# Kernel tuning notes

Hardware: AMD Instinct MI355X
Metric: run time of the kernel (lower is better)

The kernel has to match this reference:

```python
import jax, jax.numpy as jnp
import numpy as np

LAMDA = 0.05
TAU = 0.44
MARGIN = 0.05
PD_EPS = 1e-6   # torch F.pairwise_distance default eps
NORM_EPS = 1e-12  # torch F.normalize default eps

B, C = 131072, 256


def setup_inputs() -> dict:
    key = jax.random.key(0)
    k1, k2 = jax.random.split(key)
    inputs = jax.random.normal(k1, (B, C), dtype=jnp.float32)
    labels = jax.random.randint(k2, (B,), 0, C, dtype=jnp.int64)
    return {"inputs": inputs, "labels": labels}


def _hinge_loss(inputs, labels):
    # F.normalize along dim=1: x / max(||x||_2, eps)
    nrm = jnp.sqrt(jnp.sum(inputs * inputs, axis=1, keepdims=True))
    x = inputs / jnp.maximum(nrm, NORM_EPS)
    a, b = x[0::2], x[1::2]            # [B/2, C] each pair (idx, idx+1)
    # F.pairwise_distance(x,y)^2 = sum((x - y + eps)^2)
    d2 = jnp.sum((a - b + PD_EPS) ** 2, axis=1)  # [B/2]
    eq = labels[0::2] == labels[1::2]
    # Faithful to original: l starts at -1 and is STICKY once set to +1
    # (original code never resets l after a matching pair).
    l = jnp.where(jnp.cumsum(eq.astype(jnp.int32)) > 0, 1.0, -1.0)
    loss_hinge = jnp.sum(jax.nn.relu(MARGIN - l * (TAU - d2)))
    return loss_hinge  # scalar (mean of 0-d tensor == itself)


def reference(inputs, labels):
    # cross entropy with mean reduction
    logp = jax.nn.log_softmax(inputs, axis=-1)
    ce = -jnp.mean(jnp.take_along_axis(logp, labels[:, None], axis=1))
    return ce + LAMDA * _hinge_loss(inputs, labels) / 2.0
```

## Files before the change

kernel.cpp:

```cpp
#include <hip/hip_runtime.h>
#include <cstddef>

#define NROWS 131072
#define NCOLS 256
#define NPAIRS 65536
#define PBLK 512
#define PWAVES (PBLK / 64)
#define PAIRS_PER_WAVE 4
#define NBLK (NPAIRS / (PWAVES * PAIRS_PER_WAVE))
#define P0BLK 64



__device__ __forceinline__ float dpp_sum(float x) {
    x += __int_as_float(__builtin_amdgcn_update_dpp(0, __float_as_int(x), 0x121, 0xF, 0xF, false));
    x += __int_as_float(__builtin_amdgcn_update_dpp(0, __float_as_int(x), 0x122, 0xF, 0xF, false));
    x += __int_as_float(__builtin_amdgcn_update_dpp(0, __float_as_int(x), 0x124, 0xF, 0xF, false));
    x += __int_as_float(__builtin_amdgcn_update_dpp(0, __float_as_int(x), 0x128, 0xF, 0xF, false));
    x += __int_as_float(__builtin_amdgcn_update_dpp(0, __float_as_int(x), 0x142, 0xA, 0xF, false));
    x += __int_as_float(__builtin_amdgcn_update_dpp(0, __float_as_int(x), 0x143, 0xC, 0xF, false));
    return x;
}

__device__ __forceinline__ float bcast63(float x) {
    return __int_as_float(__builtin_amdgcn_readlane(__float_as_int(x), 63));
}

__device__ __forceinline__ unsigned dpp_umin(unsigned x) {
    unsigned y;
    y = (unsigned)__builtin_amdgcn_update_dpp((int)x, (int)x, 0x121, 0xF, 0xF, false); x = x < y ? x : y;
    y = (unsigned)__builtin_amdgcn_update_dpp((int)x, (int)x, 0x122, 0xF, 0xF, false); x = x < y ? x : y;
    y = (unsigned)__builtin_amdgcn_update_dpp((int)x, (int)x, 0x124, 0xF, 0xF, false); x = x < y ? x : y;
    y = (unsigned)__builtin_amdgcn_update_dpp((int)x, (int)x, 0x128, 0xF, 0xF, false); x = x < y ? x : y;
    y = (unsigned)__builtin_amdgcn_update_dpp((int)x, (int)x, 0x142, 0xA, 0xF, false); x = x < y ? x : y;
    y = (unsigned)__builtin_amdgcn_update_dpp((int)x, (int)x, 0x143, 0xC, 0xF, false); x = x < y ? x : y;
    return x;
}

__global__ __launch_bounds__(256) void dcnn_p0(const int* __restrict__ labels,
                                               unsigned* __restrict__ minslot) {
    const int t = blockIdx.x * 256 + threadIdx.x;
    const int4* L = reinterpret_cast<const int4*>(labels);
    int4 q0 = L[2 * t];
    int4 q1 = L[2 * t + 1];
    unsigned base = (unsigned)(4 * t);
    unsigned m = 0xFFFFFFFFu;
    if (q0.x == q0.y) m = base;
    if (q0.z == q0.w) { unsigned c = base + 1; m = m < c ? m : c; }
    if (q1.x == q1.y) { unsigned c = base + 2; m = m < c ? m : c; }
    if (q1.z == q1.w) { unsigned c = base + 3; m = m < c ? m : c; }
    m = dpp_umin(m);
    __shared__ unsigned wmin[4];
    if ((threadIdx.x & 63) == 63) wmin[threadIdx.x >> 6] = m;
    __syncthreads();
    if (threadIdx.x == 0) {
        unsigned a = wmin[0] < wmin[1] ? wmin[0] : wmin[1];
        unsigned b = wmin[2] < wmin[3] ? wmin[2] : wmin[3];
        minslot[blockIdx.x] = a < b ? a : b;
    }
}

__global__ __launch_bounds__(PBLK) void dcnn_pair(
    const float* __restrict__ in, const int* __restrict__ labels,
    const unsigned* __restrict__ minslot,
    float* __restrict__ ce_blk, float* __restrict__ h_blk)
{
    const int wave = threadIdx.x >> 6;
    const int lane = threadIdx.x & 63;

    unsigned p0 = dpp_umin(minslot[lane]);
    p0 = (unsigned)__builtin_amdgcn_readlane((int)p0, 63);

    const int wid = blockIdx.x * PWAVES + wave;
    float ce_acc = 0.0f, h_acc = 0.0f;

    #pragma unroll
    for (int i = 0; i < PAIRS_PER_WAVE; ++i) {
        const int p = wid * PAIRS_PER_WAVE + i;
        const float4* rowA = reinterpret_cast<const float4*>(in + (size_t)(2 * p) * NCOLS);
        const float4* rowB = reinterpret_cast<const float4*>(in + (size_t)(2 * p + 1) * NCOLS);
        float4 fa = rowA[lane];
        float4 fb = rowB[lane];
        int2 lab = reinterpret_cast<const int2*>(labels)[p];

        float sep_a = __expf(fa.x) + __expf(fa.y) + __expf(fa.z) + __expf(fa.w);
        float sep_b = __expf(fb.x) + __expf(fb.y) + __expf(fb.z) + __expf(fb.w);
        float ssp_a = fa.x * fa.x + fa.y * fa.y + fa.z * fa.z + fa.w * fa.w;
        float ssp_b = fb.x * fb.x + fb.y * fb.y + fb.z * fb.z + fb.w * fb.w;

        float sea = bcast63(dpp_sum(sep_a));
        float seb = bcast63(dpp_sum(sep_b));
        float ssa = bcast63(dpp_sum(ssp_a));
        float ssb = bcast63(dpp_sum(ssp_b));

        float inva = rsqrtf(ssa);
        float invb = rsqrtf(ssb);

        float dx = fmaf(fa.x, inva, 1e-6f - fb.x * invb);
        float dy = fmaf(fa.y, inva, 1e-6f - fb.y * invb);
        float dz = fmaf(fa.z, inva, 1e-6f - fb.z * invb);
        float dw = fmaf(fa.w, inva, 1e-6f - fb.w * invb);
        float d2p = fmaf(dx, dx, fmaf(dy, dy, fmaf(dz, dz, dw * dw)));
        float d2 = bcast63(dpp_sum(d2p));

        int sla = __builtin_amdgcn_readfirstlane(lab.x);
        int slb = __builtin_amdgcn_readfirstlane(lab.y);
        int ca = sla & 3, cb = slb & 3;
        float va_l = ca == 0 ? fa.x : ca == 1 ? fa.y : ca == 2 ? fa.z : fa.w;
        float vb_l = cb == 0 ? fb.x : cb == 1 ? fb.y : cb == 2 ? fb.z : fb.w;
        float va = __int_as_float(__builtin_amdgcn_readlane(__float_as_int(va_l), sla >> 2));
        float vb = __int_as_float(__builtin_amdgcn_readlane(__float_as_int(vb_l), slb >> 2));

        ce_acc += (__logf(sea) - va) + (__logf(seb) - vb);

        float l = ((unsigned)p >= p0) ? 1.0f : -1.0f;
        h_acc += fmaxf(0.05f - l * (0.44f - d2), 0.0f);
    }

    __shared__ float cep[PWAVES], hp[PWAVES];
    if (lane == 0) { cep[wave] = ce_acc; hp[wave] = h_acc; }
    __syncthreads();
    if (threadIdx.x == 0) {
        float c = 0.0f, h = 0.0f;
        #pragma unroll
        for (int w = 0; w < PWAVES; ++w) { c += cep[w]; h += hp[w]; }
        ce_blk[blockIdx.x] = c;
        h_blk[blockIdx.x] = h;
    }
}

__global__ __launch_bounds__(1024) void dcnn_final(const float* __restrict__ ce_blk,
                                                   const float* __restrict__ h_blk,
                                                   float* __restrict__ out) {
    const int t = threadIdx.x;
    float c = ce_blk[t] + ce_blk[t + 1024];
    float h = h_blk[t] + h_blk[t + 1024];
    c = dpp_sum(c);
    h = dpp_sum(h);
    __shared__ float cs[16], hs[16];
    if ((t & 63) == 63) { cs[t >> 6] = c; hs[t >> 6] = h; }
    __syncthreads();
    if (t == 0) {
        float C = 0.0f, H = 0.0f;
        #pragma unroll
        for (int i = 0; i < 16; ++i) { C += cs[i]; H += hs[i]; }
        out[0] = C * (1.0f / (float)NROWS) + 0.025f * H;
    }
}

extern "C" void kernel_launch(void* const* d_in, const int* in_sizes, int n_in,
                              void* d_out, int out_size, void* d_ws, size_t ws_size,
                              hipStream_t stream) {
    const float* in = (const float*)d_in[0];
    const int* labels = (const int*)d_in[1];
    float* wsf = (float*)d_ws;
    unsigned* minslot = (unsigned*)d_ws;
    float* ce_blk = wsf + 64;
    float* h_blk = wsf + 64 + NBLK;
    float* out = (float*)d_out;

    dcnn_p0<<<P0BLK, 256, 0, stream>>>(labels, minslot);
    dcnn_pair<<<NBLK, PBLK, 0, stream>>>(in, labels, minslot, ce_blk, h_blk);
    dcnn_final<<<1, 1024, 0, stream>>>(ce_blk, h_blk, out);
}
```

Baseline: 195.9 us.

## Split label gather into prelude kernel and use 16-lane groups per pair

Moves the label-logit gather into the first kernel, which now also finds the first matching pair. The main kernel then processes one pair per 16-lane group, cutting each cross-lane reduction from a full-wave DPP plus readlane to a 16-lane DPP reduction. The distance is rewritten via the dot product (2 - 2·cos plus an eps term), so the normalized difference vector is never formed. The price is an extra scattered global read per row, slightly different rounding in d2, and idle lanes in the per-pair scalar tail.

New measurement: 195.7 us. No clear change (-0.1%).

```diff
diff --git a/kernel.cpp b/kernel.cpp
--- a/kernel.cpp
+++ b/kernel.cpp
@@ -4,26 +4,27 @@
 #define NROWS 131072
 #define NCOLS 256
 #define NPAIRS 65536
-#define PBLK 512
-#define PWAVES (PBLK / 64)
-#define PAIRS_PER_WAVE 4
+#define PBLK 256
+#define PWAVES 4
+#define PITER 2
+#define PAIRS_PER_WAVE (4 * PITER)
 #define NBLK (NPAIRS / (PWAVES * PAIRS_PER_WAVE))
-#define P0BLK 64
+#define GBLK 256
 
 
-
-__device__ __forceinline__ float dpp_sum(float x) {
+__device__ __forceinline__ float rsum16(float x) {
     x += __int_as_float(__builtin_amdgcn_update_dpp(0, __float_as_int(x), 0x121, 0xF, 0xF, false));
     x += __int_as_float(__builtin_amdgcn_update_dpp(0, __float_as_int(x), 0x122, 0xF, 0xF, false));
     x += __int_as_float(__builtin_amdgcn_update_dpp(0, __float_as_int(x), 0x124, 0xF, 0xF, false));
     x += __int_as_float(__builtin_amdgcn_update_dpp(0, __float_as_int(x), 0x128, 0xF, 0xF, false));
+    return x;
+}
+
+__device__ __forceinline__ float dpp_sum(float x) {
+    x = rsum16(x);
     x += __int_as_float(__builtin_amdgcn_update_dpp(0, __float_as_int(x), 0x142, 0xA, 0xF, false));
     x += __int_as_float(__builtin_amdgcn_update_dpp(0, __float_as_int(x), 0x143, 0xC, 0xF, false));
     return x;
-}
-
-__device__ __forceinline__ float bcast63(float x) {
-    return __int_as_float(__builtin_amdgcn_readlane(__float_as_int(x), 63));
 }
 
 __device__ __forceinline__ unsigned dpp_umin(unsigned x) {
@@ -37,114 +38,139 @@
     return x;
 }
 
-__global__ __launch_bounds__(256) void dcnn_p0(const int* __restrict__ labels,
-                                               unsigned* __restrict__ minslot) {
-    const int t = blockIdx.x * 256 + threadIdx.x;
-    const int4* L = reinterpret_cast<const int4*>(labels);
-    int4 q0 = L[2 * t];
-    int4 q1 = L[2 * t + 1];
-    unsigned base = (unsigned)(4 * t);
-    unsigned m = 0xFFFFFFFFu;
-    if (q0.x == q0.y) m = base;
-    if (q0.z == q0.w) { unsigned c = base + 1; m = m < c ? m : c; }
-    if (q1.x == q1.y) { unsigned c = base + 2; m = m < c ? m : c; }
-    if (q1.z == q1.w) { unsigned c = base + 3; m = m < c ? m : c; }
+__global__ __launch_bounds__(256) void dcnn_gp0(
+    const float* __restrict__ in, const int* __restrict__ labels,
+    unsigned* __restrict__ minslot, float* __restrict__ ceg)
+{
+    const int p = blockIdx.x * 256 + threadIdx.x;
+    int2 L = reinterpret_cast<const int2*>(labels)[p];
+    float va = in[(size_t)(2 * p) * NCOLS + L.x];
+    float vb = in[(size_t)(2 * p + 1) * NCOLS + L.y];
+    float g = va + vb;
+    unsigned m = (L.x == L.y) ? (unsigned)p : 0xFFFFFFFFu;
+    g = dpp_sum(g);
     m = dpp_umin(m);
-    __shared__ unsigned wmin[4];
-    if ((threadIdx.x & 63) == 63) wmin[threadIdx.x >> 6] = m;
+    __shared__ float gs[4];
+    __shared__ unsigned ms[4];
+    const int lane = threadIdx.x & 63, w = threadIdx.x >> 6;
+    if (lane == 63) { gs[w] = g; ms[w] = m; }
     __syncthreads();
     if (threadIdx.x == 0) {
-        unsigned a = wmin[0] < wmin[1] ? wmin[0] : wmin[1];
-        unsigned b = wmin[2] < wmin[3] ? wmin[2] : wmin[3];
+        ceg[blockIdx.x] = (gs[0] + gs[1]) + (gs[2] + gs[3]);
+        unsigned a = ms[0] < ms[1] ? ms[0] : ms[1];
+        unsigned b = ms[2] < ms[3] ? ms[2] : ms[3];
         minslot[blockIdx.x] = a < b ? a : b;
     }
 }
 
 __global__ __launch_bounds__(PBLK) void dcnn_pair(
-    const float* __restrict__ in, const int* __restrict__ labels,
+    const float* __restrict__ in,
     const unsigned* __restrict__ minslot,
-    float* __restrict__ ce_blk, float* __restrict__ h_blk)
+    float* __restrict__ lse_blk, float* __restrict__ h_blk)
 {
     const int wave = threadIdx.x >> 6;
     const int lane = threadIdx.x & 63;
+    const int g = lane >> 4;
+    const int s = lane & 15;
 
-    unsigned p0 = dpp_umin(minslot[lane]);
-    p0 = (unsigned)__builtin_amdgcn_readlane((int)p0, 63);
+    unsigned m0 = minslot[lane], m1 = minslot[lane + 64];
+    unsigned m2 = minslot[lane + 128], m3 = minslot[lane + 192];
+    unsigned mm = m0 < m1 ? m0 : m1;
+    unsigned mn = m2 < m3 ? m2 : m3;
+    mm = mm < mn ? mm : mn;
+    unsigned p0 = (unsigned)__builtin_amdgcn_readlane((int)dpp_umin(mm), 63);
 
-    const int wid = blockIdx.x * PWAVES + wave;
-    float ce_acc = 0.0f, h_acc = 0.0f;
+    const int wbase = (blockIdx.x * PWAVES + wave) * PAIRS_PER_WAVE;
+    float lse_acc = 0.0f, h_acc = 0.0f;
 
     #pragma unroll
-    for (int i = 0; i < PAIRS_PER_WAVE; ++i) {
-        const int p = wid * PAIRS_PER_WAVE + i;
-        const float4* rowA = reinterpret_cast<const float4*>(in + (size_t)(2 * p) * NCOLS);
-        const float4* rowB = reinterpret_cast<const float4*>(in + (size_t)(2 * p + 1) * NCOLS);
-        float4 fa = rowA[lane];
-        float4 fb = rowB[lane];
-        int2 lab = reinterpret_cast<const int2*>(labels)[p];
+    for (int it = 0; it < PITER; ++it) {
+        const int P = wbase + it * 4 + g;
+        const float* rowa = in + (size_t)(2 * P) * NCOLS + 4 * s;
+        const float* rowb = rowa + NCOLS;
+        float4 a0 = *(const float4*)(rowa);
+        float4 b0 = *(const float4*)(rowb);
+        float4 a1 = *(const float4*)(rowa + 64);
+        float4 b1 = *(const float4*)(rowb + 64);
+        float4 a2 = *(const float4*)(rowa + 128);
+        float4 b2 = *(const float4*)(rowb + 128);
+        float4 a3 = *(const float4*)(rowa + 192);
+        float4 b3 = *(const float4*)(rowb + 192);
 
-        float sep_a = __expf(fa.x) + __expf(fa.y) + __expf(fa.z) + __expf(fa.w);
-        float sep_b = __expf(fb.x) + __expf(fb.y) + __expf(fb.z) + __expf(fb.w);
-        float ssp_a = fa.x * fa.x + fa.y * fa.y + fa.z * fa.z + fa.w * fa.w;
-        float ssp_b = fb.x * fb.x + fb.y * fb.y + fb.z * fb.z + fb.w * fb.w;
+        float ea0 = (__expf(a0.x) + __expf(a0.y)) + (__expf(a0.z) + __expf(a0.w));
+        float ea1 = (__expf(a1.x) + __expf(a1.y)) + (__expf(a1.z) + __expf(a1.w));
+        float ea2 = (__expf(a2.x) + __expf(a2.y)) + (__expf(a2.z) + __expf(a2.w));
+        float ea3 = (__expf(a3.x) + __expf(a3.y)) + (__expf(a3.z) + __expf(a3.w));
+        float se_a = (ea0 + ea1) + (ea2 + ea3);
+        float eb0 = (__expf(b0.x) + __expf(b0.y)) + (__expf(b0.z) + __expf(b0.w));
+        float eb1 = (__expf(b1.x) + __expf(b1.y)) + (__expf(b1.z) + __expf(b1.w));
+        float eb2 = (__expf(b2.x) + __expf(b2.y)) + (__expf(b2.z) + __expf(b2.w));
+        float eb3 = (__expf(b3.x) + __expf(b3.y)) + (__expf(b3.z) + __expf(b3.w));
+        float se_b = (eb0 + eb1) + (eb2 + eb3);
 
-        float sea = bcast63(dpp_sum(sep_a));
-        float seb = bcast63(dpp_sum(sep_b));
-        float ssa = bcast63(dpp_sum(ssp_a));
-        float ssb = bcast63(dpp_sum(ssp_b));
+        float sa0 = fmaf(a0.x, a0.x, fmaf(a0.y, a0.y, fmaf(a0.z, a0.z, a0.w * a0.w)));
+        float sa1 = fmaf(a1.x, a1.x, fmaf(a1.y, a1.y, fmaf(a1.z, a1.z, a1.w * a1.w)));
+        float sa2 = fmaf(a2.x, a2.x, fmaf(a2.y, a2.y, fmaf(a2.z, a2.z, a2.w * a2.w)));
+        float sa3 = fmaf(a3.x, a3.x, fmaf(a3.y, a3.y, fmaf(a3.z, a3.z, a3.w * a3.w)));
+        float ssa = (sa0 + sa1) + (sa2 + sa3);
+        float sb0 = fmaf(b0.x, b0.x, fmaf(b0.y, b0.y, fmaf(b0.z, b0.z, b0.w * b0.w)));
+        float sb1 = fmaf(b1.x, b1.x, fmaf(b1.y, b1.y, fmaf(b1.z, b1.z, b1.w * b1.w)));
+        float sb2 = fmaf(b2.x, b2.x, fmaf(b2.y, b2.y, fmaf(b2.z, b2.z, b2.w * b2.w)));
+        float sb3 = fmaf(b3.x, b3.x, fmaf(b3.y, b3.y, fmaf(b3.z, b3.z, b3.w * b3.w)));
+        float ssb = (sb0 + sb1) + (sb2 + sb3);
+        float dt0 = fmaf(a0.x, b0.x, fmaf(a0.y, b0.y, fmaf(a0.z, b0.z, a0.w * b0.w)));
+        float dt1 = fmaf(a1.x, b1.x, fmaf(a1.y, b1.y, fmaf(a1.z, b1.z, a1.w * b1.w)));
+        float dt2 = fmaf(a2.x, b2.x, fmaf(a2.y, b2.y, fmaf(a2.z, b2.z, a2.w * b2.w)));
+        float dt3 = fmaf(a3.x, b3.x, fmaf(a3.y, b3.y, fmaf(a3.z, b3.z, a3.w * b3.w)));
+        float dot = (dt0 + dt1) + (dt2 + dt3);
 
-        float inva = rsqrtf(ssa);
-        float invb = rsqrtf(ssb);
+        se_a = rsum16(se_a);
+        se_b = rsum16(se_b);
+        ssa = rsum16(ssa);
+        ssb = rsum16(ssb);
+        dot = rsum16(dot);
 
-        float dx = fmaf(fa.x, inva, 1e-6f - fb.x * invb);
-        float dy = fmaf(fa.y, inva, 1e-6f - fb.y * invb);
-        float dz = fmaf(fa.z, inva, 1e-6f - fb.z * invb);
-        float dw = fmaf(fa.w, inva, 1e-6f - fb.w * invb);
-        float d2p = fmaf(dx, dx, fmaf(dy, dy, fmaf(dz, dz, dw * dw)));
-        float d2 = bcast63(dpp_sum(d2p));
-
-        int sla = __builtin_amdgcn_readfirstlane(lab.x);
-        int slb = __builtin_amdgcn_readfirstlane(lab.y);
-        int ca = sla & 3, cb = slb & 3;
-        float va_l = ca == 0 ? fa.x : ca == 1 ? fa.y : ca == 2 ? fa.z : fa.w;
-        float vb_l = cb == 0 ? fb.x : cb == 1 ? fb.y : cb == 2 ? fb.z : fb.w;
-        float va = __int_as_float(__builtin_amdgcn_readlane(__float_as_int(va_l), sla >> 2));
-        float vb = __int_as_float(__builtin_amdgcn_readlane(__float_as_int(vb_l), slb >> 2));
-
-        ce_acc += (__logf(sea) - va) + (__logf(seb) - vb);
-
-        float l = ((unsigned)p >= p0) ? 1.0f : -1.0f;
-        h_acc += fmaxf(0.05f - l * (0.44f - d2), 0.0f);
+        if (s == 0) {
+            lse_acc += __logf(se_a) + __logf(se_b);
+            float inva = rsqrtf(ssa);
+            float invb = rsqrtf(ssb);
+            float d2 = 2.0f + 2.56e-10f - 2.0f * dot * inva * invb;
+            float l = ((unsigned)P >= p0) ? 1.0f : -1.0f;
+            h_acc += fmaxf(0.05f - l * (0.44f - d2), 0.0f);
+        }
     }
 
-    __shared__ float cep[PWAVES], hp[PWAVES];
-    if (lane == 0) { cep[wave] = ce_acc; hp[wave] = h_acc; }
+    __shared__ float lw[PWAVES * 4], hw[PWAVES * 4];
+    if (s == 0) { lw[wave * 4 + g] = lse_acc; hw[wave * 4 + g] = h_acc; }
     __syncthreads();
     if (threadIdx.x == 0) {
         float c = 0.0f, h = 0.0f;
         #pragma unroll
-        for (int w = 0; w < PWAVES; ++w) { c += cep[w]; h += hp[w]; }
-        ce_blk[blockIdx.x] = c;
+        for (int i = 0; i < PWAVES * 4; ++i) { c += lw[i]; h += hw[i]; }
+        lse_blk[blockIdx.x] = c;
         h_blk[blockIdx.x] = h;
     }
 }
 
-__global__ __launch_bounds__(1024) void dcnn_final(const float* __restrict__ ce_blk,
-                                                   const float* __restrict__ h_blk,
-                                                   float* __restrict__ out) {
+__global__ __launch_bounds__(1024) void dcnn_final(
+    const float* __restrict__ lse_blk, const float* __restrict__ h_blk,
+    const float* __restrict__ ceg, float* __restrict__ out)
+{
     const int t = threadIdx.x;
-    float c = ce_blk[t] + ce_blk[t + 1024];
+    float c = lse_blk[t] + lse_blk[t + 1024];
     float h = h_blk[t] + h_blk[t + 1024];
+    float gv = (t < GBLK) ? ceg[t] : 0.0f;
     c = dpp_sum(c);
     h = dpp_sum(h);
-    __shared__ float cs[16], hs[16];
-    if ((t & 63) == 63) { cs[t >> 6] = c; hs[t >> 6] = h; }
+    gv = dpp_sum(gv);
+    __shared__ float cs[16], hs[16], gs[16];
+    if ((t & 63) == 63) { cs[t >> 6] = c; hs[t >> 6] = h; gs[t >> 6] = gv; }
     __syncthreads();
     if (t == 0) {
-        float C = 0.0f, H = 0.0f;
+        float C = 0.0f, H = 0.0f, G = 0.0f;
         #pragma unroll
-        for (int i = 0; i < 16; ++i) { C += cs[i]; H += hs[i]; }
-        out[0] = C * (1.0f / (float)NROWS) + 0.025f * H;
+        for (int i = 0; i < 16; ++i) { C += cs[i]; H += hs[i]; G += gs[i]; }
+        out[0] = (C - G) * (1.0f / (float)NROWS) + 0.025f * H;
     }
 }
 
@@ -155,11 +181,12 @@
     const int* labels = (const int*)d_in[1];
     float* wsf = (float*)d_ws;
     unsigned* minslot = (unsigned*)d_ws;
-    float* ce_blk = wsf + 64;
-    float* h_blk = wsf + 64 + NBLK;
+    float* ceg = wsf + 256;
+    float* lse_blk = wsf + 512;
+    float* h_blk = wsf + 512 + NBLK;
     float* out = (float*)d_out;
 
-    dcnn_p0<<<P0BLK, 256, 0, stream>>>(labels, minslot);
-    dcnn_pair<<<NBLK, PBLK, 0, stream>>>(in, labels, minslot, ce_blk, h_blk);
-    dcnn_final<<<1, 1024, 0, stream>>>(ce_blk, h_blk, out);
+    dcnn_gp0<<<GBLK, 256, 0, stream>>>(in, labels, minslot, ceg);
+    dcnn_pair<<<NBLK, PBLK, 0, stream>>>(in, minslot, lse_blk, h_blk);
+    dcnn_final<<<1, 1024, 0, stream>>>(lse_blk, h_blk, ceg, out);
 }
```
